# Optimization experiments

Hardware: AMD Instinct MI355X
Metric: run time of the kernel (lower is better)

Reference implementation:

```python
import jax, jax.numpy as jnp
import numpy as np

B, M, N, T = 16, 16, 32, 80


def setup_inputs() -> dict:
    key = jax.random.key(0)
    ks = jax.random.split(key, 20)
    p = lambda k, shp: jax.random.normal(k, shp, jnp.float32) * 0.05
    return {
        "ego_traj": jax.random.normal(ks[0], (B, M, T, 6), jnp.float32),
        "ego_encoding": jax.random.normal(ks[1], (B, 256), jnp.float32),
        "agents_traj": jax.random.normal(ks[2], (B, M, N, T, 3), jnp.float32),
        "agents_states": jax.random.normal(ks[3], (B, N, 11), jnp.float32),
        # interaction_feature_encoder: Linear(10,64) -> ReLU -> Linear(64,256)
        "enc_w1": p(ks[4], (10, 64)), "enc_b1": p(ks[5], (64,)),
        "enc_w2": p(ks[6], (64, 256)), "enc_b2": p(ks[7], (256,)),
        # interaction_feature_decoder: Linear(256,64) -> ELU -> Linear(64,4) -> Sigmoid
        "dec_w1": p(ks[8], (256, 64)), "dec_b1": p(ks[9], (64,)),
        "dec_w2": p(ks[10], (64, 4)), "dec_b2": p(ks[11], (4,)),
        # weights_decoder: Linear(256,64) -> ELU -> Linear(64,8) -> Softplus
        "wd_w1": p(ks[12], (256, 64)), "wd_b1": p(ks[13], (64,)),
        "wd_w2": p(ks[14], (64, 8)), "wd_b2": p(ks[15], (8,)),
        "timesteps": 80,
    }


def reference(ego_traj, ego_encoding, agents_traj, agents_states,
              enc_w1, enc_b1, enc_w2, enc_b2,
              dec_w1, dec_b1, dec_w2, dec_b2,
              wd_w1, wd_b1, wd_w2, wd_b2, timesteps):
    Tm = timesteps
    # ---- hardcoded ego features: B,M,4 ----
    speed = ego_traj[:, :, :Tm, 3]
    acc = ego_traj[:, :, :Tm, 4]
    jerk = jnp.diff(acc, axis=-1) / 0.1
    jerk = jnp.concatenate([jerk[:, :, :1], jerk], axis=-1)
    curvature = ego_traj[:, :, :Tm, 5]
    lat_acc = speed ** 2 * curvature
    hard = jnp.stack([
        -jnp.clip(speed.mean(-1), 0.0, 15.0) / 15.0,
        jnp.clip(jnp.abs(acc).mean(-1), 0.0, 4.0) / 4.0,
        jnp.clip(jnp.abs(jerk).mean(-1), 0.0, 6.0) / 6.0,
        jnp.clip(jnp.abs(lat_acc).mean(-1), 0.0, 5.0) / 5.0,
    ], axis=-1)  # B,M,4

    # ---- latent interaction features (vectorized over M) ----
    agent_mask = (agents_states.sum(-1) != 0).astype(ego_traj.dtype)  # B,N
    ry = agents_traj[:, :, :, :Tm, 2] - ego_traj[:, :, None, :Tm, 2]  # B,M,N,T
    ry = jnp.arctan2(jnp.sin(ry), jnp.cos(ry))
    rp = agents_traj[:, :, :, :Tm, :2] - ego_traj[:, :, None, :Tm, :2]
    rp = jnp.stack([rp[..., 0] * jnp.cos(ry), rp[..., 1] * jnp.sin(ry)], axis=-1)
    av = jnp.diff(agents_traj[:, :, :, :Tm, :2], axis=-2) / 0.1
    av = jnp.concatenate([av[:, :, :, :1, :], av], axis=-2)
    evx = ego_traj[:, :, :Tm, 3] * jnp.cos(ego_traj[:, :, :Tm, 2])  # B,M,T
    evy = ego_traj[:, :, :Tm, 3] * jnp.sin(ego_traj[:, :, :Tm, 2])
    rv = jnp.stack([(av[..., 0] - evx[:, :, None]) * jnp.cos(ry),
                    (av[..., 1] - evy[:, :, None]) * jnp.sin(ry)], axis=-1)
    rel = jnp.concatenate([rp, ry[..., None], rv], axis=-1)  # B,M,N,T,5
    aattr = jnp.broadcast_to(agents_states[:, None, :, None, 6:], rel.shape[:4] + (5,))
    attr = jnp.concatenate([rel, aattr], axis=-1) * agent_mask[:, None, :, None, None]  # B,M,N,T,10
    h = jax.nn.relu(attr @ enc_w1 + enc_b1) @ enc_w2 + enc_b2  # B,M,N,T,256
    feat = h.max(axis=2).mean(axis=2)  # max over agents, mean over time -> B,M,256
    inter = jax.nn.sigmoid(jax.nn.elu(feat @ dec_w1 + dec_b1) @ dec_w2 + dec_b2)  # B,M,4

    # ---- weights (variable_cost=False -> ones_like encoding) ----
    enc_in = jnp.ones_like(ego_encoding)
    weights = jax.nn.softplus(jax.nn.elu(enc_in @ wd_w1 + wd_b1) @ wd_w2 + wd_b2)  # B,8

    # ---- collision cost: B,M ----
    dist = jnp.linalg.norm(ego_traj[:, :, None, :Tm, :2] - agents_traj[:, :, :, :Tm, :2], axis=-1)
    coll = (jnp.exp(-0.2 * dist ** 2) * agent_mask[:, None, :, None]).sum((-1, -2))

    feats = jnp.concatenate([hard, inter], axis=-1)  # B,M,8
    scores = -jnp.sum(feats * weights[:, None, :], axis=-1) - 10.0 * coll
    ego_mask = ego_traj.sum(-1).sum(-1) != 0  # B,M
    scores = jnp.where(ego_mask, scores, -jnp.inf)
    return scores, weights
```

## Files before the change

### kernel.cpp

```cpp
#include <hip/hip_runtime.h>
#include <hip/hip_fp16.h>
#include <math.h>
#include <string.h>

typedef __attribute__((ext_vector_type(8))) short short8;
typedef __attribute__((ext_vector_type(8))) _Float16 f16x8;
typedef __attribute__((ext_vector_type(2))) _Float16 h2;
typedef __attribute__((ext_vector_type(4))) float f32x4;

#define NB 16
#define NM 16
#define NN 32
#define NT 80
#define TC 10
#define NP 8

#define WS_WTS 0
#define WS_BF 16
#define WS_BB 8208
#define WS_BASE 24592
#define WS_BM_STRIDE 2112
#define WS_SC_OFF 2048

__device__ __forceinline__ short f2h(float f) {
  _Float16 h = (_Float16)f;
  short s; memcpy(&s, &h, 2); return s;
}
__device__ __forceinline__ unsigned h2bits(h2 h) {
  unsigned u; memcpy(&u, &h, 4); return u;
}

__global__ void prep_kernel(const float* __restrict__ agents_states,
                            const float* __restrict__ enc_w1,
                            const float* __restrict__ enc_b1,
                            const float* __restrict__ enc_w2,
                            const float* __restrict__ wd_w1,
                            const float* __restrict__ wd_b1,
                            const float* __restrict__ wd_w2,
                            const float* __restrict__ wd_b2,
                            float* __restrict__ ws,
                            float* __restrict__ out) {
  const int blk = blockIdx.x;
  const int tid = threadIdx.x;
  if (blk < NB) {
    __shared__ float smask[NN];
    if (tid < NN) {
      const float* st = agents_states + ((size_t)blk * NN + tid) * 11;
      float s = 0.f;
      for (int i = 0; i < 11; ++i) s += st[i];
      smask[tid] = (s != 0.f) ? 1.f : 0.f;
    }
    __syncthreads();
    h2* bb = reinterpret_cast<h2*>(ws + WS_BB) + blk * (NN * 32);
    for (int e = tid; e < NN * 32; e += 256) {
      int n = e >> 5, jp = e & 31;
      const float* st = agents_states + ((size_t)blk * NN + n) * 11 + 6;
      float v[2];
#pragma unroll
      for (int hh = 0; hh < 2; ++hh) {
        int j = jp * 2 + hh;
        float acc = st[0] * enc_w1[5 * 64 + j] + st[1] * enc_w1[6 * 64 + j] +
                    st[2] * enc_w1[7 * 64 + j] + st[3] * enc_w1[8 * 64 + j] +
                    st[4] * enc_w1[9 * 64 + j];
        v[hh] = smask[n] * acc + enc_b1[j];
      }
      h2 r; r[0] = (_Float16)v[0]; r[1] = (_Float16)v[1];
      bb[e] = r;
    }
  } else {
    __shared__ float sh[64];
    if (tid < 64) {
      float acc = wd_b1[tid];
      for (int i = 0; i < 256; ++i) acc += wd_w1[i * 64 + tid];
      sh[tid] = acc > 0.f ? acc : expm1f(acc);
    }
    __syncthreads();
    if (tid < 8) {
      float acc = wd_b2[tid];
      for (int k = 0; k < 64; ++k) acc += sh[k] * wd_w2[k * 8 + tid];
      float sp = log1pf(__expf(acc));
      ws[WS_WTS + tid] = sp;
      for (int b = 0; b < NB; ++b) out[NB * NM + b * 8 + tid] = sp;
    }
    const int g = tid >> 6;
    const int lane = tid & 63;
    short8* bft = reinterpret_cast<short8*>(ws + WS_BF);
#pragma unroll
    for (int q = 0; q < 8; ++q) {
      int s = g * 8 + q;
      int wv = s >> 3, ct = (s >> 1) & 3, kt = s & 1;
      int col = wv * 64 + ct * 16 + (lane & 15);
      int krow = (lane >> 4) * 8;
      short8 v;
#pragma unroll
      for (int j = 0; j < 8; ++j)
        v[j] = f2h(enc_w2[(kt * 32 + krow + j) * 256 + col]);
      bft[s * 64 + lane] = v;
    }
  }
}

__global__ __launch_bounds__(256, 4) void score_partial(
    const float* __restrict__ ego_traj,
    const float* __restrict__ agents_traj,
    const float* __restrict__ agents_states,
    const float* __restrict__ enc_w1,
    float* __restrict__ ws)
{
  __shared__ h2 s_rel[5][TC][NN + 1];
  __shared__ __align__(16) short s_hidden[2][NN * 64];
  __shared__ float s_ego[TC][5];
  __shared__ float s_acc[TC + 2];
  __shared__ float s_spd[TC], s_lat[TC], s_egos[TC];
  __shared__ float s_mask[NN];
  __shared__ float s_cw[4];

  const int bid = blockIdx.x;
  const int bm = bid >> 3;
  const int p = bid & 7;
  const int t0 = p * TC;
  const int b = bm >> 4;
  const int tid = threadIdx.x;
  const int lane = tid & 63;
  const int wv = tid >> 6;

  float* ws_bm = ws + WS_BASE + (size_t)bm * WS_BM_STRIDE;

  if (tid < TC) {
    int i = tid;
    const float* e = ego_traj + ((size_t)bm * NT + (t0 + i)) * 6;
    float ex = e[0], ey = e[1], eh = e[2], spd = e[3], acc = e[4], cur = e[5];
    s_ego[i][0] = ex; s_ego[i][1] = ey; s_ego[i][2] = eh;
    s_ego[i][3] = spd * __cosf(eh);
    s_ego[i][4] = spd * __sinf(eh);
    s_spd[i] = spd;
    s_acc[i + 1] = acc;
    s_lat[i] = fabsf(spd * spd * cur);
    s_egos[i] = ex + ey + eh + spd + acc + cur;
  } else if (tid == TC) {
    int tp = (p == 0) ? 0 : (t0 - 1);
    s_acc[0] = ego_traj[((size_t)bm * NT + tp) * 6 + 4];
  } else if (tid >= 64 && tid < 64 + NN) {
    int n = tid - 64;
    const float* st = agents_states + ((size_t)b * NN + n) * 11;
    float s = 0.f;
    for (int i = 0; i < 11; ++i) s += st[i];
    s_mask[n] = (s != 0.f) ? 1.f : 0.f;
  }

  const int jq = tid & 15;
  const int nh = tid >> 4;
  const int na = nh, nb_ = nh + 16;
  const int j0 = jq * 4;

  f16x8 Bf[4][2];
  {
    const f16x8* bft = reinterpret_cast<const f16x8*>(ws + WS_BF);
#pragma unroll
    for (int ct = 0; ct < 4; ++ct)
#pragma unroll
      for (int kt = 0; kt < 2; ++kt)
        Bf[ct][kt] = bft[((wv * 4 + ct) * 2 + kt) * 64 + lane];
  }

  h2 w1h[5][2];
#pragma unroll
  for (int f = 0; f < 5; ++f)
#pragma unroll
    for (int jp = 0; jp < 2; ++jp) {
      h2 r;
      r[0] = (_Float16)enc_w1[f * 64 + j0 + jp * 2];
      r[1] = (_Float16)enc_w1[f * 64 + j0 + jp * 2 + 1];
      w1h[f][jp] = r;
    }

  h2 baseA2[2], baseB2[2];
  {
    const h2* bb = reinterpret_cast<const h2*>(ws + WS_BB) + b * (NN * 32);
    baseA2[0] = bb[na * 32 + jq * 2];
    baseA2[1] = bb[na * 32 + jq * 2 + 1];
    baseB2[0] = bb[nb_ * 32 + jq * 2];
    baseB2[1] = bb[nb_ * 32 + jq * 2 + 1];
  }
  __syncthreads();

  {
    float collacc = 0.f;
    const float* atraj = agents_traj + (size_t)bm * (NN * NT * 3);
#pragma unroll
    for (int k = 0; k < 2; ++k) {
      int pp = tid + k * 256;
      if (pp < NN * TC) {
        int n = pp / TC;
        int i = pp - n * TC;
        int tg = t0 + i;
        const float* bp = atraj + n * (NT * 3) + tg * 3;
        float ax = bp[0], ay = bp[1], ah = bp[2];
        float avx, avy;
        if (tg == 0) { avx = (bp[3] - ax) * 10.f; avy = (bp[4] - ay) * 10.f; }
        else         { avx = (ax - bp[-3]) * 10.f; avy = (ay - bp[-2]) * 10.f; }
        float ex = s_ego[i][0], ey = s_ego[i][1], eh = s_ego[i][2];
        float evx = s_ego[i][3], evy = s_ego[i][4];
        float m = s_mask[n];
        float ryr = ah - eh;
        float w = ryr - 6.283185307179586f * rintf(ryr * 0.15915494309189535f);
        float cy = __cosf(ryr), sy = __sinf(ryr);
        float dx = ax - ex, dy = ay - ey;
        float r0 = dx * cy * m, r1 = dy * sy * m, r2 = w * m;
        float r3 = (avx - evx) * cy * m, r4 = (avy - evy) * sy * m;
        h2 v0, v1, v2, v3, v4;
        v0[0] = v0[1] = (_Float16)r0;
        v1[0] = v1[1] = (_Float16)r1;
        v2[0] = v2[1] = (_Float16)r2;
        v3[0] = v3[1] = (_Float16)r3;
        v4[0] = v4[1] = (_Float16)r4;
        s_rel[0][i][n] = v0;
        s_rel[1][i][n] = v1;
        s_rel[2][i][n] = v2;
        s_rel[3][i][n] = v3;
        s_rel[4][i][n] = v4;
        collacc += __expf(-0.2f * (dx * dx + dy * dy)) * m;
      }
    }
#pragma unroll
    for (int off = 1; off < 64; off <<= 1) collacc += __shfl_xor(collacc, off);
    if (lane == 0) s_cw[wv] = collacc;
  }

  if (tid >= 251) {
    int which = tid - 251;
    float s = 0.f;
    if (which == 0)      { for (int i = 0; i < TC; ++i) s += s_spd[i]; }
    else if (which == 1) { for (int i = 0; i < TC; ++i) s += fabsf(s_acc[i + 1]); }
    else if (which == 2) {
      for (int i = 0; i < TC; ++i) {
        int ia = (p == 0 && i == 0) ? 2 : (i + 1);
        s += fabsf((s_acc[ia] - s_acc[ia - 1]) * 10.f);
      }
    }
    else if (which == 3) { for (int i = 0; i < TC; ++i) s += s_lat[i]; }
    else                 { for (int i = 0; i < TC; ++i) s += s_egos[i]; }
    ws_bm[WS_SC_OFF + p * 8 + which] = s;
  }

  const int wbyteA = (na * 128 + jq * 8) ^ ((na & 7) << 4);
  const int wbyteB = (nb_ * 128 + jq * 8) ^ ((nb_ & 7) << 4);
  int abyte[2][2];
  {
    int nbl = lane & 15;
    int kb = (lane >> 4) * 16;
#pragma unroll
    for (int rt = 0; rt < 2; ++rt) {
      int row = rt * 16 + nbl;
#pragma unroll
      for (int kt = 0; kt < 2; ++kt)
        abyte[rt][kt] = (row * 128 + kt * 64 + kb) ^ ((row & 7) << 4);
    }
  }

  h2 z2; z2[0] = z2[1] = (_Float16)0.f;

  auto compute_hidden = [&](int i, int buf) {
    h2 ra0 = s_rel[0][i][na], ra1 = s_rel[1][i][na], ra2 = s_rel[2][i][na],
       ra3 = s_rel[3][i][na], ra4 = s_rel[4][i][na];
    h2 rb0 = s_rel[0][i][nb_], rb1 = s_rel[1][i][nb_], rb2 = s_rel[2][i][nb_],
       rb3 = s_rel[3][i][nb_], rb4 = s_rel[4][i][nb_];
    uint2 ua, ub;
#pragma unroll
    for (int jp = 0; jp < 2; ++jp) {
      h2 ha = baseA2[jp];
      ha = ra0 * w1h[0][jp] + ha;
      ha = ra1 * w1h[1][jp] + ha;
      ha = ra2 * w1h[2][jp] + ha;
      ha = ra3 * w1h[3][jp] + ha;
      ha = ra4 * w1h[4][jp] + ha;
      ha = __builtin_elementwise_max(ha, z2);
      h2 hb2 = baseB2[jp];
      hb2 = rb0 * w1h[0][jp] + hb2;
      hb2 = rb1 * w1h[1][jp] + hb2;
      hb2 = rb2 * w1h[2][jp] + hb2;
      hb2 = rb3 * w1h[3][jp] + hb2;
      hb2 = rb4 * w1h[4][jp] + hb2;
      hb2 = __builtin_elementwise_max(hb2, z2);
      if (jp == 0) { ua.x = h2bits(ha); ub.x = h2bits(hb2); }
      else         { ua.y = h2bits(ha); ub.y = h2bits(hb2); }
    }
    char* hb = reinterpret_cast<char*>(&s_hidden[buf][0]);
    *reinterpret_cast<uint2*>(hb + wbyteA) = ua;
    *reinterpret_cast<uint2*>(hb + wbyteB) = ub;
  };

  float macc[4] = {0.f, 0.f, 0.f, 0.f};

  auto mfma_step = [&](int buf) {
    const char* hb = reinterpret_cast<const char*>(&s_hidden[buf][0]);
    f16x8 a00 = *reinterpret_cast<const f16x8*>(hb + abyte[0][0]);
    f16x8 a01 = *reinterpret_cast<const f16x8*>(hb + abyte[0][1]);
    f16x8 a10 = *reinterpret_cast<const f16x8*>(hb + abyte[1][0]);
    f16x8 a11 = *reinterpret_cast<const f16x8*>(hb + abyte[1][1]);
#pragma unroll
    for (int ct = 0; ct < 4; ++ct) {
      f32x4 c0 = {0.f, 0.f, 0.f, 0.f}, c1 = {0.f, 0.f, 0.f, 0.f};
      c0 = __builtin_amdgcn_mfma_f32_16x16x32_f16(a00, Bf[ct][0], c0, 0, 0, 0);
      c0 = __builtin_amdgcn_mfma_f32_16x16x32_f16(a01, Bf[ct][1], c0, 0, 0, 0);
      c1 = __builtin_amdgcn_mfma_f32_16x16x32_f16(a10, Bf[ct][0], c1, 0, 0, 0);
      c1 = __builtin_amdgcn_mfma_f32_16x16x32_f16(a11, Bf[ct][1], c1, 0, 0, 0);
      float v = fmaxf(fmaxf(fmaxf(c0[0], c1[0]), fmaxf(c0[1], c1[1])),
                      fmaxf(fmaxf(c0[2], c1[2]), fmaxf(c0[3], c1[3])));
      v = fmaxf(v, __shfl_xor(v, 16));
      v = fmaxf(v, __shfl_xor(v, 32));
      macc[ct] += v;
    }
  };

  __syncthreads();
  compute_hidden(0, 0);
  __syncthreads();

  for (int i = 0; i < TC; ++i) {
    const int buf = i & 1;
    if (i + 1 < TC) compute_hidden(i + 1, buf ^ 1);
    mfma_step(buf);
    __syncthreads();
  }

  if (lane < 16) {
#pragma unroll
    for (int ct = 0; ct < 4; ++ct)
      ws_bm[p * 256 + wv * 64 + ct * 16 + lane] = macc[ct];
  }
  if (tid == 0)
    ws_bm[WS_SC_OFF + p * 8 + 5] = s_cw[0] + s_cw[1] + s_cw[2] + s_cw[3];
}

__global__ void combine_kernel(const float* __restrict__ ws,
                               const float* __restrict__ enc_b2,
                               const float* __restrict__ dec_w1,
                               const float* __restrict__ dec_b1,
                               const float* __restrict__ dec_w2,
                               const float* __restrict__ dec_b2,
                               float* __restrict__ out_scores) {
  __shared__ float s_feat[256];
  __shared__ float s_dh[64];
  __shared__ float s_hard[4];
  __shared__ float s_inter[4];
  __shared__ float s_mc[2];
  const int bm = blockIdx.x;
  const int tid = threadIdx.x;
  const float* wb = ws + WS_BASE + (size_t)bm * WS_BM_STRIDE;

  for (int c = tid; c < 256; c += 64) {
    float f = 0.f;
#pragma unroll
    for (int pp = 0; pp < NP; ++pp) f += wb[pp * 256 + c];
    s_feat[c] = f * (1.f / NT) + enc_b2[c];
  }
  const float* sc = wb + WS_SC_OFF;
  if (tid < 6) {
    float s = 0.f;
#pragma unroll
    for (int pp = 0; pp < NP; ++pp) s += sc[pp * 8 + tid];
    if (tid == 0) s_hard[0] = -fminf(fmaxf(s * (1.f / NT), 0.f), 15.f) * (1.f / 15.f);
    if (tid == 1) s_hard[1] = fminf(fmaxf(s * (1.f / NT), 0.f), 4.f) * 0.25f;
    if (tid == 2) s_hard[2] = fminf(fmaxf(s * (1.f / NT), 0.f), 6.f) * (1.f / 6.f);
    if (tid == 3) s_hard[3] = fminf(fmaxf(s * (1.f / NT), 0.f), 5.f) * 0.2f;
    if (tid == 4) s_mc[0] = s;
    if (tid == 5) s_mc[1] = s;
  }
  __syncthreads();

  {
    float a0 = 0.f, a1 = 0.f, a2 = 0.f, a3 = 0.f;
    for (int i = 0; i < 256; i += 4) {
      a0 += s_feat[i + 0] * dec_w1[(i + 0) * 64 + tid];
      a1 += s_feat[i + 1] * dec_w1[(i + 1) * 64 + tid];
      a2 += s_feat[i + 2] * dec_w1[(i + 2) * 64 + tid];
      a3 += s_feat[i + 3] * dec_w1[(i + 3) * 64 + tid];
    }
    float acc = dec_b1[tid] + ((a0 + a1) + (a2 + a3));
    s_dh[tid] = acc > 0.f ? acc : expm1f(acc);
  }
  __syncthreads();

  if (tid < 4) {
    float acc = dec_b2[tid];
    for (int k = 0; k < 64; ++k) acc += s_dh[k] * dec_w2[k * 4 + tid];
    s_inter[tid] = 1.f / (1.f + __expf(-acc));
  }
  __syncthreads();

  if (tid == 0) {
    const float* wts = ws + WS_WTS;
    float scv = 0.f;
#pragma unroll
    for (int i = 0; i < 4; ++i) scv += s_hard[i] * wts[i];
#pragma unroll
    for (int i = 0; i < 4; ++i) scv += s_inter[i] * wts[4 + i];
    scv = -scv - 10.f * s_mc[1];
    if (s_mc[0] == 0.f) scv = -INFINITY;
    out_scores[bm] = scv;
  }
}

extern "C" void kernel_launch(void* const* d_in, const int* in_sizes, int n_in,
                              void* d_out, int out_size, void* d_ws, size_t ws_size,
                              hipStream_t stream) {
  const float* ego_traj      = (const float*)d_in[0];
  const float* agents_traj   = (const float*)d_in[2];
  const float* agents_states = (const float*)d_in[3];
  const float* enc_w1 = (const float*)d_in[4];
  const float* enc_b1 = (const float*)d_in[5];
  const float* enc_w2 = (const float*)d_in[6];
  const float* enc_b2 = (const float*)d_in[7];
  const float* dec_w1 = (const float*)d_in[8];
  const float* dec_b1 = (const float*)d_in[9];
  const float* dec_w2 = (const float*)d_in[10];
  const float* dec_b2 = (const float*)d_in[11];
  const float* wd_w1 = (const float*)d_in[12];
  const float* wd_b1 = (const float*)d_in[13];
  const float* wd_w2 = (const float*)d_in[14];
  const float* wd_b2 = (const float*)d_in[15];

  float* out = (float*)d_out;
  float* ws = (float*)d_ws;

  prep_kernel<<<NB + 1, 256, 0, stream>>>(agents_states, enc_w1, enc_b1, enc_w2,
                                          wd_w1, wd_b1, wd_w2, wd_b2, ws, out);
  score_partial<<<NB * NM * NP, 256, 0, stream>>>(
      ego_traj, agents_traj, agents_states, enc_w1, ws);
  combine_kernel<<<NB * NM, 64, 0, stream>>>(
      ws, enc_b2, dec_w1, dec_b1, dec_w2, dec_b2, out);
}
```

Measured before the change: 45.96 us.

## Fuse score partial and combine kernels into one block per trajectory

Replaces the time-split score kernel (8 blocks per b,m) and the separate combine kernel with one 256-thread block per (b,m) that processes all 80 timesteps and computes the decoder and final score in place. The MFMA is restructured so that rows are 16 timesteps per agent slab, with a running max over agents computed across the 32 agent slabs. Relative features are packed into h4/h2 shared arrays. This removes one launch and the workspace round-trip, in exchange for only 256 blocks with a large shared footprint, which lowers parallelism and occupancy.

```diff
diff --git a/kernel.cpp b/kernel.cpp
--- a/kernel.cpp
+++ b/kernel.cpp
@@ -5,6 +5,7 @@
 
 typedef __attribute__((ext_vector_type(8))) short short8;
 typedef __attribute__((ext_vector_type(8))) _Float16 f16x8;
+typedef __attribute__((ext_vector_type(4))) _Float16 h4;
 typedef __attribute__((ext_vector_type(2))) _Float16 h2;
 typedef __attribute__((ext_vector_type(4))) float f32x4;
 
@@ -12,15 +13,11 @@
 #define NM 16
 #define NN 32
 #define NT 80
-#define TC 10
-#define NP 8
+#define NTILE 5
 
 #define WS_WTS 0
 #define WS_BF 16
 #define WS_BB 8208
-#define WS_BASE 24592
-#define WS_BM_STRIDE 2112
-#define WS_SC_OFF 2048
 
 __device__ __forceinline__ short f2h(float f) {
   _Float16 h = (_Float16)f;
@@ -88,8 +85,8 @@
 #pragma unroll
     for (int q = 0; q < 8; ++q) {
       int s = g * 8 + q;
-      int wv = s >> 3, ct = (s >> 1) & 3, kt = s & 1;
-      int col = wv * 64 + ct * 16 + (lane & 15);
+      int wv = s >> 3, jb = (s >> 1) & 3, kt = s & 1;
+      int col = wv * 64 + jb * 16 + (lane & 15);
       int krow = (lane >> 4) * 8;
       short8 v;
 #pragma unroll
@@ -100,48 +97,50 @@
   }
 }
 
-__global__ __launch_bounds__(256, 4) void score_partial(
+__global__ __launch_bounds__(256, 1) void score_kernel(
     const float* __restrict__ ego_traj,
     const float* __restrict__ agents_traj,
     const float* __restrict__ agents_states,
     const float* __restrict__ enc_w1,
-    float* __restrict__ ws)
+    const float* __restrict__ enc_b2,
+    const float* __restrict__ dec_w1, const float* __restrict__ dec_b1,
+    const float* __restrict__ dec_w2, const float* __restrict__ dec_b2,
+    const float* __restrict__ ws,
+    float* __restrict__ out_scores)
 {
-  __shared__ h2 s_rel[5][TC][NN + 1];
-  __shared__ __align__(16) short s_hidden[2][NN * 64];
-  __shared__ float s_ego[TC][5];
-  __shared__ float s_acc[TC + 2];
-  __shared__ float s_spd[TC], s_lat[TC], s_egos[TC];
+  __shared__ h4 s_r01[NT][NN + 1];
+  __shared__ h4 s_r23[NT][NN + 1];
+  __shared__ h2 s_r4[NT][NN + 1];
+  __shared__ __align__(16) char s_hid[NN * 16 * 64 * 2];
+  __shared__ float s_ego[NT][5];
+  __shared__ float s_acc[NT], s_spd[NT], s_lat[NT], s_egos[NT];
   __shared__ float s_mask[NN];
   __shared__ float s_cw[4];
-
-  const int bid = blockIdx.x;
-  const int bm = bid >> 3;
-  const int p = bid & 7;
-  const int t0 = p * TC;
+  __shared__ float s_feat[256];
+  __shared__ float s_dhp[4][64];
+  __shared__ float s_dh[64];
+  __shared__ float s_hard[4], s_inter[4];
+  __shared__ float s_egosum, s_coll;
+
+  const int bm = blockIdx.x;
   const int b = bm >> 4;
   const int tid = threadIdx.x;
   const int lane = tid & 63;
   const int wv = tid >> 6;
 
-  float* ws_bm = ws + WS_BASE + (size_t)bm * WS_BM_STRIDE;
-
-  if (tid < TC) {
-    int i = tid;
-    const float* e = ego_traj + ((size_t)bm * NT + (t0 + i)) * 6;
+  if (tid < NT) {
+    int t = tid;
+    const float* e = ego_traj + ((size_t)bm * NT + t) * 6;
     float ex = e[0], ey = e[1], eh = e[2], spd = e[3], acc = e[4], cur = e[5];
-    s_ego[i][0] = ex; s_ego[i][1] = ey; s_ego[i][2] = eh;
-    s_ego[i][3] = spd * __cosf(eh);
-    s_ego[i][4] = spd * __sinf(eh);
-    s_spd[i] = spd;
-    s_acc[i + 1] = acc;
-    s_lat[i] = fabsf(spd * spd * cur);
-    s_egos[i] = ex + ey + eh + spd + acc + cur;
-  } else if (tid == TC) {
-    int tp = (p == 0) ? 0 : (t0 - 1);
-    s_acc[0] = ego_traj[((size_t)bm * NT + tp) * 6 + 4];
-  } else if (tid >= 64 && tid < 64 + NN) {
-    int n = tid - 64;
+    s_ego[t][0] = ex; s_ego[t][1] = ey; s_ego[t][2] = eh;
+    s_ego[t][3] = spd * __cosf(eh);
+    s_ego[t][4] = spd * __sinf(eh);
+    s_spd[t] = spd;
+    s_acc[t] = acc;
+    s_lat[t] = fabsf(spd * spd * cur);
+    s_egos[t] = ex + ey + eh + spd + acc + cur;
+  } else if (tid >= 128 && tid < 128 + NN) {
+    int n = tid - 128;
     const float* st = agents_states + ((size_t)b * NN + n) * 11;
     float s = 0.f;
     for (int i = 0; i < 11; ++i) s += st[i];
@@ -157,10 +156,10 @@
   {
     const f16x8* bft = reinterpret_cast<const f16x8*>(ws + WS_BF);
 #pragma unroll
-    for (int ct = 0; ct < 4; ++ct)
+    for (int jb = 0; jb < 4; ++jb)
 #pragma unroll
       for (int kt = 0; kt < 2; ++kt)
-        Bf[ct][kt] = bft[((wv * 4 + ct) * 2 + kt) * 64 + lane];
+        Bf[jb][kt] = bft[((wv * 4 + jb) * 2 + kt) * 64 + lane];
   }
 
   h2 w1h[5][2];
@@ -188,217 +187,176 @@
     float collacc = 0.f;
     const float* atraj = agents_traj + (size_t)bm * (NN * NT * 3);
 #pragma unroll
-    for (int k = 0; k < 2; ++k) {
+    for (int k = 0; k < 10; ++k) {
       int pp = tid + k * 256;
-      if (pp < NN * TC) {
-        int n = pp / TC;
-        int i = pp - n * TC;
-        int tg = t0 + i;
-        const float* bp = atraj + n * (NT * 3) + tg * 3;
-        float ax = bp[0], ay = bp[1], ah = bp[2];
-        float avx, avy;
-        if (tg == 0) { avx = (bp[3] - ax) * 10.f; avy = (bp[4] - ay) * 10.f; }
-        else         { avx = (ax - bp[-3]) * 10.f; avy = (ay - bp[-2]) * 10.f; }
-        float ex = s_ego[i][0], ey = s_ego[i][1], eh = s_ego[i][2];
-        float evx = s_ego[i][3], evy = s_ego[i][4];
-        float m = s_mask[n];
-        float ryr = ah - eh;
-        float w = ryr - 6.283185307179586f * rintf(ryr * 0.15915494309189535f);
-        float cy = __cosf(ryr), sy = __sinf(ryr);
-        float dx = ax - ex, dy = ay - ey;
-        float r0 = dx * cy * m, r1 = dy * sy * m, r2 = w * m;
-        float r3 = (avx - evx) * cy * m, r4 = (avy - evy) * sy * m;
-        h2 v0, v1, v2, v3, v4;
-        v0[0] = v0[1] = (_Float16)r0;
-        v1[0] = v1[1] = (_Float16)r1;
-        v2[0] = v2[1] = (_Float16)r2;
-        v3[0] = v3[1] = (_Float16)r3;
-        v4[0] = v4[1] = (_Float16)r4;
-        s_rel[0][i][n] = v0;
-        s_rel[1][i][n] = v1;
-        s_rel[2][i][n] = v2;
-        s_rel[3][i][n] = v3;
-        s_rel[4][i][n] = v4;
-        collacc += __expf(-0.2f * (dx * dx + dy * dy)) * m;
-      }
+      int n = pp / NT;
+      int t = pp - n * NT;
+      const float* bp = atraj + n * (NT * 3) + t * 3;
+      float ax = bp[0], ay = bp[1], ah = bp[2];
+      float avx, avy;
+      if (t == 0) { avx = (bp[3] - ax) * 10.f; avy = (bp[4] - ay) * 10.f; }
+      else        { avx = (ax - bp[-3]) * 10.f; avy = (ay - bp[-2]) * 10.f; }
+      float ex = s_ego[t][0], ey = s_ego[t][1], eh = s_ego[t][2];
+      float evx = s_ego[t][3], evy = s_ego[t][4];
+      float m = s_mask[n];
+      float ryr = ah - eh;
+      float w = ryr - 6.283185307179586f * rintf(ryr * 0.15915494309189535f);
+      float cy = __cosf(ryr), sy = __sinf(ryr);
+      float dx = ax - ex, dy = ay - ey;
+      float r0 = dx * cy * m, r1 = dy * sy * m, r2 = w * m;
+      float r3 = (avx - evx) * cy * m, r4 = (avy - evy) * sy * m;
+      h4 v01, v23; h2 v4;
+      v01[0] = v01[1] = (_Float16)r0; v01[2] = v01[3] = (_Float16)r1;
+      v23[0] = v23[1] = (_Float16)r2; v23[2] = v23[3] = (_Float16)r3;
+      v4[0] = v4[1] = (_Float16)r4;
+      s_r01[t][n] = v01;
+      s_r23[t][n] = v23;
+      s_r4[t][n] = v4;
+      collacc += __expf(-0.2f * (dx * dx + dy * dy)) * m;
     }
 #pragma unroll
     for (int off = 1; off < 64; off <<= 1) collacc += __shfl_xor(collacc, off);
     if (lane == 0) s_cw[wv] = collacc;
   }
-
-  if (tid >= 251) {
-    int which = tid - 251;
+  __syncthreads();
+
+  const int tl = lane & 15, kg = lane >> 4;
+  const int sw_r = (tl & 7) << 4;
+  const int aoff0 = tl * 128 + (((0 << 6) | (kg << 4)) ^ sw_r);
+  const int aoff1 = tl * 128 + (((1 << 6) | (kg << 4)) ^ sw_r);
+
+  h2 z2; z2[0] = z2[1] = (_Float16)0.f;
+  float macc[4] = {0.f, 0.f, 0.f, 0.f};
+
+  for (int tile = 0; tile < NTILE; ++tile) {
+    const int tbase = tile * 16;
+#pragma unroll 4
+    for (int tt = 0; tt < 16; ++tt) {
+      const int gt = tbase + tt;
+      h4 a01 = s_r01[gt][na], a23 = s_r23[gt][na];
+      h2 a4 = s_r4[gt][na];
+      h4 c01 = s_r01[gt][nb_], c23 = s_r23[gt][nb_];
+      h2 c4 = s_r4[gt][nb_];
+      h2 a0 = __builtin_shufflevector(a01, a01, 0, 1);
+      h2 a1 = __builtin_shufflevector(a01, a01, 2, 3);
+      h2 a2 = __builtin_shufflevector(a23, a23, 0, 1);
+      h2 a3 = __builtin_shufflevector(a23, a23, 2, 3);
+      h2 c0 = __builtin_shufflevector(c01, c01, 0, 1);
+      h2 c1 = __builtin_shufflevector(c01, c01, 2, 3);
+      h2 c2 = __builtin_shufflevector(c23, c23, 0, 1);
+      h2 c3 = __builtin_shufflevector(c23, c23, 2, 3);
+      uint2 ua, ub;
+#pragma unroll
+      for (int jp = 0; jp < 2; ++jp) {
+        h2 ha = baseA2[jp];
+        ha = a0 * w1h[0][jp] + ha;
+        ha = a1 * w1h[1][jp] + ha;
+        ha = a2 * w1h[2][jp] + ha;
+        ha = a3 * w1h[3][jp] + ha;
+        ha = a4 * w1h[4][jp] + ha;
+        ha = __builtin_elementwise_max(ha, z2);
+        h2 hb = baseB2[jp];
+        hb = c0 * w1h[0][jp] + hb;
+        hb = c1 * w1h[1][jp] + hb;
+        hb = c2 * w1h[2][jp] + hb;
+        hb = c3 * w1h[3][jp] + hb;
+        hb = c4 * w1h[4][jp] + hb;
+        hb = __builtin_elementwise_max(hb, z2);
+        if (jp == 0) { ua.x = h2bits(ha); ub.x = h2bits(hb); }
+        else         { ua.y = h2bits(ha); ub.y = h2bits(hb); }
+      }
+      const int swz = (tt & 7) << 4;
+      *reinterpret_cast<uint2*>(s_hid + na * 2048 + tt * 128 + ((jq * 8) ^ swz)) = ua;
+      *reinterpret_cast<uint2*>(s_hid + nb_ * 2048 + tt * 128 + ((jq * 8) ^ swz)) = ub;
+    }
+    __syncthreads();
+
+    f32x4 rmax[4];
+#pragma unroll
+    for (int jb = 0; jb < 4; ++jb)
+      rmax[jb] = f32x4{-3e38f, -3e38f, -3e38f, -3e38f};
+#pragma unroll 4
+    for (int n = 0; n < NN; ++n) {
+      const char* slab = s_hid + n * 2048;
+      f16x8 A0 = *reinterpret_cast<const f16x8*>(slab + aoff0);
+      f16x8 A1 = *reinterpret_cast<const f16x8*>(slab + aoff1);
+#pragma unroll
+      for (int jb = 0; jb < 4; ++jb) {
+        f32x4 c = {0.f, 0.f, 0.f, 0.f};
+        c = __builtin_amdgcn_mfma_f32_16x16x32_f16(A0, Bf[jb][0], c, 0, 0, 0);
+        c = __builtin_amdgcn_mfma_f32_16x16x32_f16(A1, Bf[jb][1], c, 0, 0, 0);
+        rmax[jb] = __builtin_elementwise_max(rmax[jb], c);
+      }
+    }
+#pragma unroll
+    for (int jb = 0; jb < 4; ++jb) {
+      float s = (rmax[jb][0] + rmax[jb][1]) + (rmax[jb][2] + rmax[jb][3]);
+      s += __shfl_xor(s, 16);
+      s += __shfl_xor(s, 32);
+      macc[jb] += s;
+    }
+    __syncthreads();
+  }
+
+  if (lane < 16) {
+#pragma unroll
+    for (int jb = 0; jb < 4; ++jb) {
+      int col = wv * 64 + jb * 16 + lane;
+      s_feat[col] = macc[jb] * (1.f / NT) + enc_b2[col];
+    }
+  }
+  if (tid >= 248 && tid < 253) {
+    int which = tid - 248;
     float s = 0.f;
-    if (which == 0)      { for (int i = 0; i < TC; ++i) s += s_spd[i]; }
-    else if (which == 1) { for (int i = 0; i < TC; ++i) s += fabsf(s_acc[i + 1]); }
-    else if (which == 2) {
-      for (int i = 0; i < TC; ++i) {
-        int ia = (p == 0 && i == 0) ? 2 : (i + 1);
-        s += fabsf((s_acc[ia] - s_acc[ia - 1]) * 10.f);
-      }
-    }
-    else if (which == 3) { for (int i = 0; i < TC; ++i) s += s_lat[i]; }
-    else                 { for (int i = 0; i < TC; ++i) s += s_egos[i]; }
-    ws_bm[WS_SC_OFF + p * 8 + which] = s;
-  }
-
-  const int wbyteA = (na * 128 + jq * 8) ^ ((na & 7) << 4);
-  const int wbyteB = (nb_ * 128 + jq * 8) ^ ((nb_ & 7) << 4);
-  int abyte[2][2];
+    if (which == 0)      { for (int t = 0; t < NT; ++t) s += s_spd[t];
+                           s_hard[0] = -fminf(fmaxf(s * (1.f / NT), 0.f), 15.f) * (1.f / 15.f); }
+    else if (which == 1) { for (int t = 0; t < NT; ++t) s += fabsf(s_acc[t]);
+                           s_hard[1] = fminf(fmaxf(s * (1.f / NT), 0.f), 4.f) * 0.25f; }
+    else if (which == 2) { for (int t = 0; t < NT; ++t) {
+                             int th = t ? t : 1;
+                             s += fabsf((s_acc[th] - s_acc[th - 1]) * 10.f);
+                           }
+                           s_hard[2] = fminf(fmaxf(s * (1.f / NT), 0.f), 6.f) * (1.f / 6.f); }
+    else if (which == 3) { for (int t = 0; t < NT; ++t) s += s_lat[t];
+                           s_hard[3] = fminf(fmaxf(s * (1.f / NT), 0.f), 5.f) * 0.2f; }
+    else                 { for (int t = 0; t < NT; ++t) s += s_egos[t];
+                           s_egosum = s; }
+  }
+  __syncthreads();
+
   {
-    int nbl = lane & 15;
-    int kb = (lane >> 4) * 16;
-#pragma unroll
-    for (int rt = 0; rt < 2; ++rt) {
-      int row = rt * 16 + nbl;
-#pragma unroll
-      for (int kt = 0; kt < 2; ++kt)
-        abyte[rt][kt] = (row * 128 + kt * 64 + kb) ^ ((row & 7) << 4);
-    }
-  }
-
-  h2 z2; z2[0] = z2[1] = (_Float16)0.f;
-
-  auto compute_hidden = [&](int i, int buf) {
-    h2 ra0 = s_rel[0][i][na], ra1 = s_rel[1][i][na], ra2 = s_rel[2][i][na],
-       ra3 = s_rel[3][i][na], ra4 = s_rel[4][i][na];
-    h2 rb0 = s_rel[0][i][nb_], rb1 = s_rel[1][i][nb_], rb2 = s_rel[2][i][nb_],
-       rb3 = s_rel[3][i][nb_], rb4 = s_rel[4][i][nb_];
-    uint2 ua, ub;
-#pragma unroll
-    for (int jp = 0; jp < 2; ++jp) {
-      h2 ha = baseA2[jp];
-      ha = ra0 * w1h[0][jp] + ha;
-      ha = ra1 * w1h[1][jp] + ha;
-      ha = ra2 * w1h[2][jp] + ha;
-      ha = ra3 * w1h[3][jp] + ha;
-      ha = ra4 * w1h[4][jp] + ha;
-      ha = __builtin_elementwise_max(ha, z2);
-      h2 hb2 = baseB2[jp];
-      hb2 = rb0 * w1h[0][jp] + hb2;
-      hb2 = rb1 * w1h[1][jp] + hb2;
-      hb2 = rb2 * w1h[2][jp] + hb2;
-      hb2 = rb3 * w1h[3][jp] + hb2;
-      hb2 = rb4 * w1h[4][jp] + hb2;
-      hb2 = __builtin_elementwise_max(hb2, z2);
-      if (jp == 0) { ua.x = h2bits(ha); ub.x = h2bits(hb2); }
-      else         { ua.y = h2bits(ha); ub.y = h2bits(hb2); }
-    }
-    char* hb = reinterpret_cast<char*>(&s_hidden[buf][0]);
-    *reinterpret_cast<uint2*>(hb + wbyteA) = ua;
-    *reinterpret_cast<uint2*>(hb + wbyteB) = ub;
-  };
-
-  float macc[4] = {0.f, 0.f, 0.f, 0.f};
-
-  auto mfma_step = [&](int buf) {
-    const char* hb = reinterpret_cast<const char*>(&s_hidden[buf][0]);
-    f16x8 a00 = *reinterpret_cast<const f16x8*>(hb + abyte[0][0]);
-    f16x8 a01 = *reinterpret_cast<const f16x8*>(hb + abyte[0][1]);
-    f16x8 a10 = *reinterpret_cast<const f16x8*>(hb + abyte[1][0]);
-    f16x8 a11 = *reinterpret_cast<const f16x8*>(hb + abyte[1][1]);
-#pragma unroll
-    for (int ct = 0; ct < 4; ++ct) {
-      f32x4 c0 = {0.f, 0.f, 0.f, 0.f}, c1 = {0.f, 0.f, 0.f, 0.f};
-      c0 = __builtin_amdgcn_mfma_f32_16x16x32_f16(a00, Bf[ct][0], c0, 0, 0, 0);
-      c0 = __builtin_amdgcn_mfma_f32_16x16x32_f16(a01, Bf[ct][1], c0, 0, 0, 0);
-      c1 = __builtin_amdgcn_mfma_f32_16x16x32_f16(a10, Bf[ct][0], c1, 0, 0, 0);
-      c1 = __builtin_amdgcn_mfma_f32_16x16x32_f16(a11, Bf[ct][1], c1, 0, 0, 0);
-      float v = fmaxf(fmaxf(fmaxf(c0[0], c1[0]), fmaxf(c0[1], c1[1])),
-                      fmaxf(fmaxf(c0[2], c1[2]), fmaxf(c0[3], c1[3])));
-      v = fmaxf(v, __shfl_xor(v, 16));
-      v = fmaxf(v, __shfl_xor(v, 32));
-      macc[ct] += v;
-    }
-  };
-
-  __syncthreads();
-  compute_hidden(0, 0);
-  __syncthreads();
-
-  for (int i = 0; i < TC; ++i) {
-    const int buf = i & 1;
-    if (i + 1 < TC) compute_hidden(i + 1, buf ^ 1);
-    mfma_step(buf);
-    __syncthreads();
-  }
-
-  if (lane < 16) {
-#pragma unroll
-    for (int ct = 0; ct < 4; ++ct)
-      ws_bm[p * 256 + wv * 64 + ct * 16 + lane] = macc[ct];
-  }
-  if (tid == 0)
-    ws_bm[WS_SC_OFF + p * 8 + 5] = s_cw[0] + s_cw[1] + s_cw[2] + s_cw[3];
-}
-
-__global__ void combine_kernel(const float* __restrict__ ws,
-                               const float* __restrict__ enc_b2,
-                               const float* __restrict__ dec_w1,
-                               const float* __restrict__ dec_b1,
-                               const float* __restrict__ dec_w2,
-                               const float* __restrict__ dec_b2,
-                               float* __restrict__ out_scores) {
-  __shared__ float s_feat[256];
-  __shared__ float s_dh[64];
-  __shared__ float s_hard[4];
-  __shared__ float s_inter[4];
-  __shared__ float s_mc[2];
-  const int bm = blockIdx.x;
-  const int tid = threadIdx.x;
-  const float* wb = ws + WS_BASE + (size_t)bm * WS_BM_STRIDE;
-
-  for (int c = tid; c < 256; c += 64) {
-    float f = 0.f;
-#pragma unroll
-    for (int pp = 0; pp < NP; ++pp) f += wb[pp * 256 + c];
-    s_feat[c] = f * (1.f / NT) + enc_b2[c];
-  }
-  const float* sc = wb + WS_SC_OFF;
-  if (tid < 6) {
-    float s = 0.f;
-#pragma unroll
-    for (int pp = 0; pp < NP; ++pp) s += sc[pp * 8 + tid];
-    if (tid == 0) s_hard[0] = -fminf(fmaxf(s * (1.f / NT), 0.f), 15.f) * (1.f / 15.f);
-    if (tid == 1) s_hard[1] = fminf(fmaxf(s * (1.f / NT), 0.f), 4.f) * 0.25f;
-    if (tid == 2) s_hard[2] = fminf(fmaxf(s * (1.f / NT), 0.f), 6.f) * (1.f / 6.f);
-    if (tid == 3) s_hard[3] = fminf(fmaxf(s * (1.f / NT), 0.f), 5.f) * 0.2f;
-    if (tid == 4) s_mc[0] = s;
-    if (tid == 5) s_mc[1] = s;
-  }
-  __syncthreads();
-
-  {
-    float a0 = 0.f, a1 = 0.f, a2 = 0.f, a3 = 0.f;
-    for (int i = 0; i < 256; i += 4) {
-      a0 += s_feat[i + 0] * dec_w1[(i + 0) * 64 + tid];
-      a1 += s_feat[i + 1] * dec_w1[(i + 1) * 64 + tid];
-      a2 += s_feat[i + 2] * dec_w1[(i + 2) * 64 + tid];
-      a3 += s_feat[i + 3] * dec_w1[(i + 3) * 64 + tid];
-    }
-    float acc = dec_b1[tid] + ((a0 + a1) + (a2 + a3));
+    const int q = tid >> 6, j = tid & 63;
+    float a = 0.f;
+#pragma unroll 4
+    for (int i = 0; i < 64; ++i)
+      a += s_feat[q * 64 + i] * dec_w1[(q * 64 + i) * 64 + j];
+    s_dhp[q][j] = a;
+  }
+  __syncthreads();
+  if (tid < 64) {
+    float acc = dec_b1[tid] + ((s_dhp[0][tid] + s_dhp[1][tid]) +
+                               (s_dhp[2][tid] + s_dhp[3][tid]));
     s_dh[tid] = acc > 0.f ? acc : expm1f(acc);
-  }
-  __syncthreads();
-
+  } else if (tid == 64) {
+    s_coll = s_cw[0] + s_cw[1] + s_cw[2] + s_cw[3];
+  }
+  __syncthreads();
   if (tid < 4) {
     float acc = dec_b2[tid];
     for (int k = 0; k < 64; ++k) acc += s_dh[k] * dec_w2[k * 4 + tid];
     s_inter[tid] = 1.f / (1.f + __expf(-acc));
   }
   __syncthreads();
-
   if (tid == 0) {
     const float* wts = ws + WS_WTS;
-    float scv = 0.f;
-#pragma unroll
-    for (int i = 0; i < 4; ++i) scv += s_hard[i] * wts[i];
-#pragma unroll
-    for (int i = 0; i < 4; ++i) scv += s_inter[i] * wts[4 + i];
-    scv = -scv - 10.f * s_mc[1];
-    if (s_mc[0] == 0.f) scv = -INFINITY;
-    out_scores[bm] = scv;
+    float sc = 0.f;
+#pragma unroll
+    for (int i = 0; i < 4; ++i) sc += s_hard[i] * wts[i];
+#pragma unroll
+    for (int i = 0; i < 4; ++i) sc += s_inter[i] * wts[4 + i];
+    sc = -sc - 10.f * s_coll;
+    if (s_egosum == 0.f) sc = -INFINITY;
+    out_scores[bm] = sc;
   }
 }
 
@@ -426,8 +384,7 @@
 
   prep_kernel<<<NB + 1, 256, 0, stream>>>(agents_states, enc_w1, enc_b1, enc_w2,
                                           wd_w1, wd_b1, wd_w2, wd_b2, ws, out);
-  score_partial<<<NB * NM * NP, 256, 0, stream>>>(
-      ego_traj, agents_traj, agents_states, enc_w1, ws);
-  combine_kernel<<<NB * NM, 64, 0, stream>>>(
-      ws, enc_b2, dec_w1, dec_b1, dec_w2, dec_b2, out);
-}
+  score_kernel<<<NB * NM, 256, 0, stream>>>(
+      ego_traj, agents_traj, agents_states, enc_w1, enc_b2,
+      dec_w1, dec_b1, dec_w2, dec_b2, ws, out);
+}
```

Measured after the change: 59.39 us. 29.2% more time.

## Put time on MFMA rows and keep the agent max in registers

Applied to the files above, without the earlier changes.

Swaps the MFMA tile orientation so the 16 rows are timesteps rather than agents. The max over agents then becomes an elementwise register max across agent chunks, which removes the per-timestep cross-lane shuffles. The time chunk grows from 10 to 16 and blocks per trajectory drop from 8 to 5, using a 2D grid. The agent base activations are staged in shared memory, and hidden tiles are computed four agents per chunk with double buffering. The cost is more shared memory per block and fewer, larger blocks, which could lower occupancy.

```diff
diff --git a/kernel.cpp b/kernel.cpp
--- a/kernel.cpp
+++ b/kernel.cpp
@@ -5,6 +5,7 @@
 
 typedef __attribute__((ext_vector_type(8))) short short8;
 typedef __attribute__((ext_vector_type(8))) _Float16 f16x8;
+typedef __attribute__((ext_vector_type(4))) _Float16 h4;
 typedef __attribute__((ext_vector_type(2))) _Float16 h2;
 typedef __attribute__((ext_vector_type(4))) float f32x4;
 
@@ -12,15 +13,17 @@
 #define NM 16
 #define NN 32
 #define NT 80
-#define TC 10
-#define NP 8
+#define TC 16
+#define NP 5
+#define CH 4
+#define NCH 8
 
 #define WS_WTS 0
 #define WS_BF 16
 #define WS_BB 8208
 #define WS_BASE 24592
-#define WS_BM_STRIDE 2112
-#define WS_SC_OFF 2048
+#define WS_BM_STRIDE 1344
+#define WS_SC_OFF 1280
 
 __device__ __forceinline__ short f2h(float f) {
   _Float16 h = (_Float16)f;
@@ -28,6 +31,9 @@
 }
 __device__ __forceinline__ unsigned h2bits(h2 h) {
   unsigned u; memcpy(&u, &h, 4); return u;
+}
+__device__ __forceinline__ h2 bits2h(unsigned u) {
+  h2 h; memcpy(&h, &u, 4); return h;
 }
 
 __global__ void prep_kernel(const float* __restrict__ agents_states,
@@ -88,8 +94,8 @@
 #pragma unroll
     for (int q = 0; q < 8; ++q) {
       int s = g * 8 + q;
-      int wv = s >> 3, ct = (s >> 1) & 3, kt = s & 1;
-      int col = wv * 64 + ct * 16 + (lane & 15);
+      int wv = s >> 3, jb = (s >> 1) & 3, kt = s & 1;
+      int col = wv * 64 + jb * 16 + (lane & 15);
       int krow = (lane >> 4) * 8;
       short8 v;
 #pragma unroll
@@ -107,17 +113,19 @@
     const float* __restrict__ enc_w1,
     float* __restrict__ ws)
 {
-  __shared__ h2 s_rel[5][TC][NN + 1];
-  __shared__ __align__(16) short s_hidden[2][NN * 64];
+  __shared__ h4 s_r01[NN][TC];
+  __shared__ h4 s_r23[NN][TC];
+  __shared__ h2 s_r4[NN][TC];
+  __shared__ uint2 s_bb[NN][16];
+  __shared__ __align__(16) char s_hid[2][CH][TC * 128];
   __shared__ float s_ego[TC][5];
   __shared__ float s_acc[TC + 2];
   __shared__ float s_spd[TC], s_lat[TC], s_egos[TC];
   __shared__ float s_mask[NN];
   __shared__ float s_cw[4];
 
-  const int bid = blockIdx.x;
-  const int bm = bid >> 3;
-  const int p = bid & 7;
+  const int p = blockIdx.x;
+  const int bm = blockIdx.y;
   const int t0 = p * TC;
   const int b = bm >> 4;
   const int tid = threadIdx.x;
@@ -147,20 +155,27 @@
     for (int i = 0; i < 11; ++i) s += st[i];
     s_mask[n] = (s != 0.f) ? 1.f : 0.f;
   }
+  {
+    const uint2* bbt = reinterpret_cast<const uint2*>(ws + WS_BB) + b * 512;
+#pragma unroll
+    for (int k = 0; k < 2; ++k) {
+      int e = tid + k * 256;
+      s_bb[e >> 4][e & 15] = bbt[e];
+    }
+  }
 
   const int jq = tid & 15;
-  const int nh = tid >> 4;
-  const int na = nh, nb_ = nh + 16;
+  const int tt = tid >> 4;
   const int j0 = jq * 4;
 
   f16x8 Bf[4][2];
   {
     const f16x8* bft = reinterpret_cast<const f16x8*>(ws + WS_BF);
 #pragma unroll
-    for (int ct = 0; ct < 4; ++ct)
+    for (int jb = 0; jb < 4; ++jb)
 #pragma unroll
       for (int kt = 0; kt < 2; ++kt)
-        Bf[ct][kt] = bft[((wv * 4 + ct) * 2 + kt) * 64 + lane];
+        Bf[jb][kt] = bft[((wv * 4 + jb) * 2 + kt) * 64 + lane];
   }
 
   h2 w1h[5][2];
@@ -173,15 +188,6 @@
       r[1] = (_Float16)enc_w1[f * 64 + j0 + jp * 2 + 1];
       w1h[f][jp] = r;
     }
-
-  h2 baseA2[2], baseB2[2];
-  {
-    const h2* bb = reinterpret_cast<const h2*>(ws + WS_BB) + b * (NN * 32);
-    baseA2[0] = bb[na * 32 + jq * 2];
-    baseA2[1] = bb[na * 32 + jq * 2 + 1];
-    baseB2[0] = bb[nb_ * 32 + jq * 2];
-    baseB2[1] = bb[nb_ * 32 + jq * 2 + 1];
-  }
   __syncthreads();
 
   {
@@ -190,37 +196,31 @@
 #pragma unroll
     for (int k = 0; k < 2; ++k) {
       int pp = tid + k * 256;
-      if (pp < NN * TC) {
-        int n = pp / TC;
-        int i = pp - n * TC;
-        int tg = t0 + i;
-        const float* bp = atraj + n * (NT * 3) + tg * 3;
-        float ax = bp[0], ay = bp[1], ah = bp[2];
-        float avx, avy;
-        if (tg == 0) { avx = (bp[3] - ax) * 10.f; avy = (bp[4] - ay) * 10.f; }
-        else         { avx = (ax - bp[-3]) * 10.f; avy = (ay - bp[-2]) * 10.f; }
-        float ex = s_ego[i][0], ey = s_ego[i][1], eh = s_ego[i][2];
-        float evx = s_ego[i][3], evy = s_ego[i][4];
-        float m = s_mask[n];
-        float ryr = ah - eh;
-        float w = ryr - 6.283185307179586f * rintf(ryr * 0.15915494309189535f);
-        float cy = __cosf(ryr), sy = __sinf(ryr);
-        float dx = ax - ex, dy = ay - ey;
-        float r0 = dx * cy * m, r1 = dy * sy * m, r2 = w * m;
-        float r3 = (avx - evx) * cy * m, r4 = (avy - evy) * sy * m;
-        h2 v0, v1, v2, v3, v4;
-        v0[0] = v0[1] = (_Float16)r0;
-        v1[0] = v1[1] = (_Float16)r1;
-        v2[0] = v2[1] = (_Float16)r2;
-        v3[0] = v3[1] = (_Float16)r3;
-        v4[0] = v4[1] = (_Float16)r4;
-        s_rel[0][i][n] = v0;
-        s_rel[1][i][n] = v1;
-        s_rel[2][i][n] = v2;
-        s_rel[3][i][n] = v3;
-        s_rel[4][i][n] = v4;
-        collacc += __expf(-0.2f * (dx * dx + dy * dy)) * m;
-      }
+      int n = pp >> 4;
+      int i = pp & 15;
+      int tg = t0 + i;
+      const float* bp = atraj + n * (NT * 3) + tg * 3;
+      float ax = bp[0], ay = bp[1], ah = bp[2];
+      float avx, avy;
+      if (tg == 0) { avx = (bp[3] - ax) * 10.f; avy = (bp[4] - ay) * 10.f; }
+      else         { avx = (ax - bp[-3]) * 10.f; avy = (ay - bp[-2]) * 10.f; }
+      float ex = s_ego[i][0], ey = s_ego[i][1], eh = s_ego[i][2];
+      float evx = s_ego[i][3], evy = s_ego[i][4];
+      float m = s_mask[n];
+      float ryr = ah - eh;
+      float w = ryr - 6.283185307179586f * rintf(ryr * 0.15915494309189535f);
+      float cy = __cosf(ryr), sy = __sinf(ryr);
+      float dx = ax - ex, dy = ay - ey;
+      float r0 = dx * cy * m, r1 = dy * sy * m, r2 = w * m;
+      float r3 = (avx - evx) * cy * m, r4 = (avy - evy) * sy * m;
+      h4 v01, v23; h2 v4;
+      v01[0] = v01[1] = (_Float16)r0; v01[2] = v01[3] = (_Float16)r1;
+      v23[0] = v23[1] = (_Float16)r2; v23[2] = v23[3] = (_Float16)r3;
+      v4[0] = v4[1] = (_Float16)r4;
+      s_r01[n][i] = v01;
+      s_r23[n][i] = v23;
+      s_r4[n][i] = v4;
+      collacc += __expf(-0.2f * (dx * dx + dy * dy)) * m;
     }
 #pragma unroll
     for (int off = 1; off < 64; off <<= 1) collacc += __shfl_xor(collacc, off);
@@ -243,91 +243,82 @@
     ws_bm[WS_SC_OFF + p * 8 + which] = s;
   }
 
-  const int wbyteA = (na * 128 + jq * 8) ^ ((na & 7) << 4);
-  const int wbyteB = (nb_ * 128 + jq * 8) ^ ((nb_ & 7) << 4);
-  int abyte[2][2];
+  const int tl = lane & 15, kg = lane >> 4;
+  const int swr = (tl & 7) << 4;
+  const int aoff0 = tl * 128 + ((kg * 16) ^ swr);
+  const int aoff1 = tl * 128 + ((64 + kg * 16) ^ swr);
+  const int wbyte = tt * 128 + ((jq * 8) ^ ((tt & 7) << 4));
+
+  h2 z2; z2[0] = z2[1] = (_Float16)0.f;
+
+  auto compute_chunk = [&](int c, int buf) {
+#pragma unroll
+    for (int nn = 0; nn < CH; ++nn) {
+      const int n = c * CH + nn;
+      h4 r01 = s_r01[n][tt];
+      h4 r23 = s_r23[n][tt];
+      h2 r4 = s_r4[n][tt];
+      uint2 bb = s_bb[n][jq];
+      h2 a0 = __builtin_shufflevector(r01, r01, 0, 1);
+      h2 a1 = __builtin_shufflevector(r01, r01, 2, 3);
+      h2 a2 = __builtin_shufflevector(r23, r23, 0, 1);
+      h2 a3 = __builtin_shufflevector(r23, r23, 2, 3);
+      uint2 u;
+#pragma unroll
+      for (int jp = 0; jp < 2; ++jp) {
+        h2 ha = bits2h(jp ? bb.y : bb.x);
+        ha = a0 * w1h[0][jp] + ha;
+        ha = a1 * w1h[1][jp] + ha;
+        ha = a2 * w1h[2][jp] + ha;
+        ha = a3 * w1h[3][jp] + ha;
+        ha = r4 * w1h[4][jp] + ha;
+        ha = __builtin_elementwise_max(ha, z2);
+        if (jp == 0) u.x = h2bits(ha); else u.y = h2bits(ha);
+      }
+      *reinterpret_cast<uint2*>(&s_hid[buf][nn][0] + wbyte) = u;
+    }
+  };
+
+  f32x4 rmax[4];
+#pragma unroll
+  for (int jb = 0; jb < 4; ++jb)
+    rmax[jb] = f32x4{-3e38f, -3e38f, -3e38f, -3e38f};
+
+  auto mfma_step = [&](int buf) {
+#pragma unroll
+    for (int nn = 0; nn < CH; ++nn) {
+      const char* slab = &s_hid[buf][nn][0];
+      f16x8 A0 = *reinterpret_cast<const f16x8*>(slab + aoff0);
+      f16x8 A1 = *reinterpret_cast<const f16x8*>(slab + aoff1);
+#pragma unroll
+      for (int jb = 0; jb < 4; ++jb) {
+        f32x4 c = {0.f, 0.f, 0.f, 0.f};
+        c = __builtin_amdgcn_mfma_f32_16x16x32_f16(A0, Bf[jb][0], c, 0, 0, 0);
+        c = __builtin_amdgcn_mfma_f32_16x16x32_f16(A1, Bf[jb][1], c, 0, 0, 0);
+        rmax[jb] = __builtin_elementwise_max(rmax[jb], c);
+      }
+    }
+  };
+
+  __syncthreads();
+  compute_chunk(0, 0);
+  __syncthreads();
+
+  for (int c = 0; c < NCH; ++c) {
+    if (c + 1 < NCH) compute_chunk(c + 1, (c + 1) & 1);
+    mfma_step(c & 1);
+    __syncthreads();
+  }
+
   {
-    int nbl = lane & 15;
-    int kb = (lane >> 4) * 16;
-#pragma unroll
-    for (int rt = 0; rt < 2; ++rt) {
-      int row = rt * 16 + nbl;
-#pragma unroll
-      for (int kt = 0; kt < 2; ++kt)
-        abyte[rt][kt] = (row * 128 + kt * 64 + kb) ^ ((row & 7) << 4);
-    }
-  }
-
-  h2 z2; z2[0] = z2[1] = (_Float16)0.f;
-
-  auto compute_hidden = [&](int i, int buf) {
-    h2 ra0 = s_rel[0][i][na], ra1 = s_rel[1][i][na], ra2 = s_rel[2][i][na],
-       ra3 = s_rel[3][i][na], ra4 = s_rel[4][i][na];
-    h2 rb0 = s_rel[0][i][nb_], rb1 = s_rel[1][i][nb_], rb2 = s_rel[2][i][nb_],
-       rb3 = s_rel[3][i][nb_], rb4 = s_rel[4][i][nb_];
-    uint2 ua, ub;
-#pragma unroll
-    for (int jp = 0; jp < 2; ++jp) {
-      h2 ha = baseA2[jp];
-      ha = ra0 * w1h[0][jp] + ha;
-      ha = ra1 * w1h[1][jp] + ha;
-      ha = ra2 * w1h[2][jp] + ha;
-      ha = ra3 * w1h[3][jp] + ha;
-      ha = ra4 * w1h[4][jp] + ha;
-      ha = __builtin_elementwise_max(ha, z2);
-      h2 hb2 = baseB2[jp];
-      hb2 = rb0 * w1h[0][jp] + hb2;
-      hb2 = rb1 * w1h[1][jp] + hb2;
-      hb2 = rb2 * w1h[2][jp] + hb2;
-      hb2 = rb3 * w1h[3][jp] + hb2;
-      hb2 = rb4 * w1h[4][jp] + hb2;
-      hb2 = __builtin_elementwise_max(hb2, z2);
-      if (jp == 0) { ua.x = h2bits(ha); ub.x = h2bits(hb2); }
-      else         { ua.y = h2bits(ha); ub.y = h2bits(hb2); }
-    }
-    char* hb = reinterpret_cast<char*>(&s_hidden[buf][0]);
-    *reinterpret_cast<uint2*>(hb + wbyteA) = ua;
-    *reinterpret_cast<uint2*>(hb + wbyteB) = ub;
-  };
-
-  float macc[4] = {0.f, 0.f, 0.f, 0.f};
-
-  auto mfma_step = [&](int buf) {
-    const char* hb = reinterpret_cast<const char*>(&s_hidden[buf][0]);
-    f16x8 a00 = *reinterpret_cast<const f16x8*>(hb + abyte[0][0]);
-    f16x8 a01 = *reinterpret_cast<const f16x8*>(hb + abyte[0][1]);
-    f16x8 a10 = *reinterpret_cast<const f16x8*>(hb + abyte[1][0]);
-    f16x8 a11 = *reinterpret_cast<const f16x8*>(hb + abyte[1][1]);
-#pragma unroll
-    for (int ct = 0; ct < 4; ++ct) {
-      f32x4 c0 = {0.f, 0.f, 0.f, 0.f}, c1 = {0.f, 0.f, 0.f, 0.f};
-      c0 = __builtin_amdgcn_mfma_f32_16x16x32_f16(a00, Bf[ct][0], c0, 0, 0, 0);
-      c0 = __builtin_amdgcn_mfma_f32_16x16x32_f16(a01, Bf[ct][1], c0, 0, 0, 0);
-      c1 = __builtin_amdgcn_mfma_f32_16x16x32_f16(a10, Bf[ct][0], c1, 0, 0, 0);
-      c1 = __builtin_amdgcn_mfma_f32_16x16x32_f16(a11, Bf[ct][1], c1, 0, 0, 0);
-      float v = fmaxf(fmaxf(fmaxf(c0[0], c1[0]), fmaxf(c0[1], c1[1])),
-                      fmaxf(fmaxf(c0[2], c1[2]), fmaxf(c0[3], c1[3])));
-      v = fmaxf(v, __shfl_xor(v, 16));
-      v = fmaxf(v, __shfl_xor(v, 32));
-      macc[ct] += v;
-    }
-  };
-
-  __syncthreads();
-  compute_hidden(0, 0);
-  __syncthreads();
-
-  for (int i = 0; i < TC; ++i) {
-    const int buf = i & 1;
-    if (i + 1 < TC) compute_hidden(i + 1, buf ^ 1);
-    mfma_step(buf);
-    __syncthreads();
-  }
-
-  if (lane < 16) {
-#pragma unroll
-    for (int ct = 0; ct < 4; ++ct)
-      ws_bm[p * 256 + wv * 64 + ct * 16 + lane] = macc[ct];
+#pragma unroll
+    for (int jb = 0; jb < 4; ++jb) {
+      float s = (rmax[jb][0] + rmax[jb][1]) + (rmax[jb][2] + rmax[jb][3]);
+      s += __shfl_xor(s, 16);
+      s += __shfl_xor(s, 32);
+      if (lane < 16)
+        ws_bm[p * 256 + wv * 64 + jb * 16 + lane] = s;
+    }
   }
   if (tid == 0)
     ws_bm[WS_SC_OFF + p * 8 + 5] = s_cw[0] + s_cw[1] + s_cw[2] + s_cw[3];
@@ -426,7 +417,8 @@
 
   prep_kernel<<<NB + 1, 256, 0, stream>>>(agents_states, enc_w1, enc_b1, enc_w2,
                                           wd_w1, wd_b1, wd_w2, wd_b2, ws, out);
-  score_partial<<<NB * NM * NP, 256, 0, stream>>>(
+  dim3 grid(NP, NB * NM);
+  score_partial<<<grid, 256, 0, stream>>>(
       ego_traj, agents_traj, agents_states, enc_w1, ws);
   combine_kernel<<<NB * NM, 64, 0, stream>>>(
       ws, enc_b2, dec_w1, dec_b1, dec_w2, dec_b2, out);
```

Result: faster. 43.26 us (-5.9%).
